# Performance work log

Measured on AMD Instinct MI355X. Metric: run time of the kernel, lower is better.

The kernel has to match this reference:

```python
import jax, jax.numpy as jnp
import numpy as np


def _lstm_layer(x, h0, c0, w_ih, w_hh, b):
    """x: [T,B,I], h0/c0: [B,H], w_ih: [4H,I], w_hh: [4H,H], b: [4H]. PyTorch gate order i,f,g,o."""
    H = h0.shape[-1]
    # Precompute input projection for all timesteps in one big GEMM.
    xg = jnp.einsum('tbi,gi->tbg', x, w_ih) + b  # [T,B,4H]

    def step(carry, xg_t):
        h, c = carry
        g = xg_t + h @ w_hh.T  # [B,4H]
        i, f, gg, o = jnp.split(g, 4, axis=-1)
        c_new = jax.nn.sigmoid(f) * c + jax.nn.sigmoid(i) * jnp.tanh(gg)
        h_new = jax.nn.sigmoid(o) * jnp.tanh(c_new)
        return (h_new, c_new), h_new

    (_, _), hs = jax.lax.scan(step, (h0, c0), xg)
    return hs  # [T,B,H]


def setup_inputs() -> dict:
    key = jax.random.key(0)
    ks = jax.random.split(key, 12)
    T, B, I, H, O, L = 2048, 32, 256, 512, 1024, 2
    s = 1.0 / np.sqrt(H)  # PyTorch LSTM init scale
    return {
        'x': jax.random.normal(ks[0], (T, B, I), jnp.float32),
        'h0': jnp.zeros((L, B, H), jnp.float32),
        'c0': jnp.zeros((L, B, H), jnp.float32),
        'w_ih0': jax.random.normal(ks[1], (4 * H, I), jnp.float32) * s,
        'w_hh0': jax.random.normal(ks[2], (4 * H, H), jnp.float32) * s,
        'b_ih0': jax.random.normal(ks[3], (4 * H,), jnp.float32) * s,
        'b_hh0': jax.random.normal(ks[4], (4 * H,), jnp.float32) * s,
        'w_ih1': jax.random.normal(ks[5], (4 * H, H), jnp.float32) * s,
        'w_hh1': jax.random.normal(ks[6], (4 * H, H), jnp.float32) * s,
        'b_ih1': jax.random.normal(ks[7], (4 * H,), jnp.float32) * s,
        'b_hh1': jax.random.normal(ks[8], (4 * H,), jnp.float32) * s,
        'fc_w': jax.random.normal(ks[9], (O, H), jnp.float32) * s,
        'fc_b': jax.random.normal(ks[10], (O,), jnp.float32) * s,
    }


def reference(x, h0, c0, w_ih0, w_hh0, b_ih0, b_hh0, w_ih1, w_hh1, b_ih1, b_hh1, fc_w, fc_b):
    h1 = _lstm_layer(x, h0[0], c0[0], w_ih0, w_hh0, b_ih0 + b_hh0)   # [T,B,H]
    h2 = _lstm_layer(h1, h0[1], c0[1], w_ih1, w_hh1, b_ih1 + b_hh1)  # [T,B,H]
    logits = h2[-1] @ fc_w.T + fc_b  # out[-1] -> fc, [B,O]
    return jax.nn.log_softmax(logits, axis=1)
```

## Files before the change

### kernel.cpp

```cpp
#include <hip/hip_runtime.h>
#include <stdint.h>

#define TT 2048
#define BB 32
#define II 256
#define HH 512
#define OO 1024
#define NWGL 64
#define NWG 128
#define RING 32

typedef __attribute__((ext_vector_type(8))) short short8;
typedef __attribute__((ext_vector_type(4))) float floatx4;

__device__ __forceinline__ unsigned short f2bf(float f) {
  union { float f; unsigned u; } v; v.f = f;
  unsigned r = v.u + 0x7FFFu + ((v.u >> 16) & 1u);
  return (unsigned short)(r >> 16);
}
__device__ __forceinline__ float bf2f(unsigned short b) {
  union { float f; unsigned u; } v; v.u = ((unsigned)b) << 16; return v.f;
}
__device__ __forceinline__ float sigmf(float x) { return 1.0f / (1.0f + __expf(-x)); }
__device__ __forceinline__ float tanhfast(float x) {
  float xc = fminf(fmaxf(x, -15.f), 15.f);
  float e = __expf(2.f * xc);
  return (e - 1.f) / (e + 1.f);
}

#define LD1(d, va, IMM)                                                     \
  asm volatile("global_load_dwordx4 %0, %1, off offset:" IMM " sc0 sc1"     \
               : "=v"(d) : "v"(va) : "memory")
#define LD1C(d, va, IMM)                                                    \
  asm volatile("global_load_dwordx4 %0, %1, off offset:" IMM                \
               : "=v"(d) : "v"(va) : "memory")

#define ISSUE8(dst, va) do {                                                \
    LD1(dst[0], va, "0");   LD1(dst[1], va, "64");                          \
    LD1(dst[2], va, "128"); LD1(dst[3], va, "192");                         \
    LD1(dst[4], va, "256"); LD1(dst[5], va, "320");                         \
    LD1(dst[6], va, "384"); LD1(dst[7], va, "448"); } while (0)
#define ISSUE8C(dst, va) do {                                               \
    LD1C(dst[0], va, "0");   LD1C(dst[1], va, "64");                        \
    LD1C(dst[2], va, "128"); LD1C(dst[3], va, "192");                       \
    LD1C(dst[4], va, "256"); LD1C(dst[5], va, "320");                       \
    LD1C(dst[6], va, "384"); LD1C(dst[7], va, "448"); } while (0)

#define WAITV(N) do {                                                       \
    asm volatile("s_waitcnt vmcnt(" #N ")" ::: "memory");                   \
    __builtin_amdgcn_sched_barrier(0); } while (0)

#define MF8(tt_, src, wbase) do {                                           \
    _Pragma("unroll")                                                       \
    for (int j = 0; j < 8; j++) {                                           \
      acc[0][tt_] = __builtin_amdgcn_mfma_f32_16x16x32_bf16(src[j], wf[0][(wbase) + j], acc[0][tt_], 0, 0, 0); \
      acc[1][tt_] = __builtin_amdgcn_mfma_f32_16x16x32_bf16(src[j], wf[1][(wbase) + j], acc[1][tt_], 0, 0, 0); \
    } } while (0)

#define PROGREAD(dst, addr64)                                               \
  asm volatile("global_load_dword %0, %1, off sc0 sc1"                      \
               : "=v"(dst) : "v"(addr64) : "memory")

#define BARRIER(gcnt, root, gen, target, do_poll) do {                      \
  if (lane == 0) {                                                          \
    int prev = __hip_atomic_fetch_add(gcnt, 1, __ATOMIC_RELAXED, __HIP_MEMORY_SCOPE_AGENT); \
    if (prev == 8 * (target) - 1) {                                         \
      int p2 = __hip_atomic_fetch_add(root, 1, __ATOMIC_RELAXED, __HIP_MEMORY_SCOPE_AGENT); \
      if (p2 == 8 * (target) - 1) {                                         \
        __hip_atomic_store(gen, (target), __ATOMIC_RELAXED, __HIP_MEMORY_SCOPE_AGENT); \
      } else if (do_poll) {                                                 \
        while (__hip_atomic_load(gen, __ATOMIC_RELAXED, __HIP_MEMORY_SCOPE_AGENT) < (target)) \
          __builtin_amdgcn_s_sleep(1);                                      \
      }                                                                     \
    } else if (do_poll) {                                                   \
      while (__hip_atomic_load(gen, __ATOMIC_RELAXED, __HIP_MEMORY_SCOPE_AGENT) < (target)) \
        __builtin_amdgcn_s_sleep(1);                                        \
    }                                                                       \
  } } while (0)

#define TAIL(hwaddr) do {                                                   \
  _Pragma("unroll")                                                         \
  for (int tau = 0; tau < 2; tau++) {                                       \
    _Pragma("unroll")                                                       \
    for (int tt = 0; tt < 2; tt++) {                                        \
      _Pragma("unroll")                                                     \
      for (int r = 0; r < 4; r++) {                                         \
        float val = acc[tau][tt][r];                                        \
        float nl = (gate == 2) ? tanhfast(val) : sigmf(val);                \
        int base2 = (lane & 48) | u;                                        \
        float iv = __shfl(nl, base2);                                       \
        float fv = __shfl(nl, base2 | 4);                                   \
        float gv = __shfl(nl, base2 | 8);                                   \
        float ov = __shfl(nl, base2 | 12);                                  \
        if (gate == 0) {                                                    \
          float cn = fv * cst[tau][tt][r] + iv * gv;                        \
          cst[tau][tt][r] = cn;                                             \
          float hn = ov * tanhfast(cn);                                     \
          int b = tt * 16 + krow * 4 + r;                                   \
          sh[b][tau * 4 + u] = f2bf(hn);                                    \
        }                                                                   \
      }                                                                     \
    }                                                                       \
  }                                                                         \
  asm volatile("s_waitcnt lgkmcnt(0)" ::: "memory");                        \
  __builtin_amdgcn_sched_barrier(0);                                        \
  if (lane < 32) {                                                          \
    short8 v = *reinterpret_cast<const short8*>(&sh[lane][0]);              \
    unsigned long long sa = (hwaddr) + stoff;                               \
    asm volatile("global_store_dwordx4 %0, %1, off sc0 sc1"                 \
                 :: "v"(sa), "v"(v) : "memory");                            \
  } } while (0)

__global__ void k_convert_x(const float* __restrict__ x, ushort* __restrict__ xb, int n4) {
  int i = blockIdx.x * blockDim.x + threadIdx.x;
  int stride = gridDim.x * blockDim.x;
  const float4* xf = reinterpret_cast<const float4*>(x);
  ushort4* ob = reinterpret_cast<ushort4*>(xb);
  for (; i < n4; i += stride) {
    float4 f = xf[i];
    ushort4 o;
    o.x = f2bf(f.x); o.y = f2bf(f.y); o.z = f2bf(f.z); o.w = f2bf(f.w);
    ob[i] = o;
  }
}

__global__ void k_init(const float* __restrict__ h0in, ushort* __restrict__ ring,
                       ushort* __restrict__ h1b1, int* __restrict__ bar) {
  int i = threadIdx.x;
  ushort* slot31 = ring + (RING - 1) * BB * HH;
  for (int k = i; k < BB * HH; k += blockDim.x) {
    slot31[k] = f2bf(h0in[k]);
    h1b1[k]   = f2bf(h0in[BB * HH + k]);
  }
  for (int k = i; k < 1024; k += blockDim.x) bar[k] = 0;
}

__global__ __launch_bounds__(64, 1) void k_lstm(
    const ushort* __restrict__ xb,
    const float* __restrict__ w_ih0, const float* __restrict__ w_hh0,
    const float* __restrict__ b_ih0, const float* __restrict__ b_hh0,
    const float* __restrict__ w_ih1, const float* __restrict__ w_hh1,
    const float* __restrict__ b_ih1, const float* __restrict__ b_hh1,
    const float* __restrict__ c0in,
    ushort* __restrict__ ring,
    ushort* __restrict__ h1b0, ushort* __restrict__ h1b1,
    int* __restrict__ bar)
{
  __shared__ ushort sh[BB][8];
  const int wg = blockIdx.x;
  const int lane = threadIdx.x;
  const bool isL0 = wg < NWGL;
  const int g = isL0 ? wg : wg - NWGL;
  const int col = lane & 15;
  const int krow = lane >> 4;
  const int u = col & 3;
  const int gate = col >> 2;

  short8 wf[2][32];
#define LOADW(dst, base, rowlen, kbase, tau) do {                             \
    const int _grow = gate * HH + g * 8 + (tau) * 4 + u;                      \
    const float* _p = (base) + (size_t)_grow * (rowlen) + (kbase) + krow * 8; \
    short8 _r;                                                                \
    _Pragma("unroll")                                                         \
    for (int _j = 0; _j < 8; _j++) _r[_j] = (short)f2bf(_p[_j]);              \
    (dst) = _r; } while (0)

  if (isL0) {
#pragma unroll
    for (int tau = 0; tau < 2; tau++) {
#pragma unroll
      for (int kk = 0; kk < 8; kk++)  LOADW(wf[tau][kk],      w_ih0, II, kk * 32, tau);
#pragma unroll
      for (int kk = 0; kk < 16; kk++) LOADW(wf[tau][8 + kk],  w_hh0, HH, kk * 32, tau);
    }
  } else {
#pragma unroll
    for (int tau = 0; tau < 2; tau++) {
#pragma unroll
      for (int kk = 0; kk < 16; kk++) LOADW(wf[tau][kk],      w_ih1, HH, kk * 32, tau);
#pragma unroll
      for (int kk = 0; kk < 16; kk++) LOADW(wf[tau][16 + kk], w_hh1, HH, kk * 32, tau);
    }
  }
  float bias[2];
#pragma unroll
  for (int tau = 0; tau < 2; tau++) {
    const int grow = gate * HH + g * 8 + tau * 4 + u;
    bias[tau] = isL0 ? (b_ih0[grow] + b_hh0[grow]) : (b_ih1[grow] + b_hh1[grow]);
  }

  float cst[2][2][4];
  {
    const float* cbase = c0in + (isL0 ? 0 : 1) * BB * HH;
#pragma unroll
    for (int tau = 0; tau < 2; tau++)
#pragma unroll
      for (int tt = 0; tt < 2; tt++)
#pragma unroll
        for (int r = 0; r < 4; r++) {
          int b = tt * 16 + krow * 4 + r;
          cst[tau][tt][r] = cbase[b * HH + g * 8 + tau * 4 + u];
        }
  }

  int* gcnt = bar + (isL0 ? 0 : 320) + (g >> 3) * 32;
  int* root = bar + (isL0 ? 256 : 576);
  int* gen  = bar + (isL0 ? 288 : 608);
  const unsigned long long genOther =
      (unsigned long long)(bar + (isL0 ? 608 : 288));

  const int vo00 = col * 1024 + krow * 16;
  const unsigned long long stoff = (unsigned long long)(lane * 1024 + g * 16);
  ushort* h1bufs[2] = { h1b0, h1b1 };

  short8 wa[8], wb[8], wc[8], wd[8];
  floatx4 acc[2][2];
  const floatx4 bi0 = (floatx4){ bias[0], bias[0], bias[0], bias[0] };
  const floatx4 bi1 = (floatx4){ bias[1], bias[1], bias[1], bias[1] };

  if (isL0) {
    const unsigned long long xbase = (unsigned long long)xb + (col * 512 + krow * 16);
    int seen1 = 0;
    for (int t = 0; t < TT; ++t) {
      if (((t & 7) == 0) && t >= 32) {
        while (seen1 < t - 24) {
          int sv; PROGREAD(sv, genOther); WAITV(0); seen1 = sv;
          if (seen1 < t - 24) __builtin_amdgcn_s_sleep(8);
        }
      }
      acc[0][0] = bi0; acc[0][1] = bi0; acc[1][0] = bi1; acc[1][1] = bi1;
      const unsigned long long ha =
          (unsigned long long)ring + ((t + RING - 1) & (RING - 1)) * (BB * HH * 2) + vo00;
      const unsigned long long xa = xbase + (unsigned long long)t * (BB * II * 2);
      ISSUE8(wa, ha); ISSUE8(wb, ha + 512); ISSUE8(wc, ha + 16384); ISSUE8(wd, ha + 16896);
      WAITV(24); MF8(0, wa, 8);  ISSUE8C(wa, xa);
      WAITV(24); MF8(0, wb, 16); ISSUE8C(wb, xa + 8192);
      WAITV(24); MF8(1, wc, 8);
      WAITV(16); MF8(1, wd, 16);
      WAITV(8);  MF8(0, wa, 0);
      WAITV(0);  MF8(1, wb, 0);
      const unsigned long long hw =
          (unsigned long long)ring + (t & (RING - 1)) * (BB * HH * 2);
      TAIL(hw);
      WAITV(0);
      BARRIER(gcnt, root, gen, t + 1, (t != TT - 1));
    }
  } else {
    int seen0 = 0;
    int sv_next = 0;
    for (int t = 0; t < TT; ++t) {
      acc[0][0] = bi0; acc[0][1] = bi0; acc[1][0] = bi1; acc[1][1] = bi1;
      const unsigned long long h1a =
          (unsigned long long)h1bufs[(t + 1) & 1] + vo00;
      ISSUE8(wa, h1a); ISSUE8(wb, h1a + 512); ISSUE8(wc, h1a + 16384); ISSUE8(wd, h1a + 16896);
      if (seen0 < t + 1) {
        while (true) {
          int sv; PROGREAD(sv, genOther); WAITV(0); seen0 = sv;
          if (seen0 >= t + 1) break;
          __builtin_amdgcn_s_sleep(8);
        }
      }
      const unsigned long long h0a =
          (unsigned long long)ring + (t & (RING - 1)) * (BB * HH * 2) + vo00;
      WAITV(24); MF8(0, wa, 16); ISSUE8(wa, h0a);
      WAITV(24); MF8(0, wb, 24); ISSUE8(wb, h0a + 512);
      WAITV(24); MF8(1, wc, 16); ISSUE8(wc, h0a + 16384);
      WAITV(24); MF8(1, wd, 24); ISSUE8(wd, h0a + 16896);
      WAITV(24); MF8(0, wa, 0);
      WAITV(16); MF8(0, wb, 8);
      WAITV(8);  MF8(1, wc, 0);
      WAITV(0);  MF8(1, wd, 8);
      const unsigned long long hw = (unsigned long long)h1bufs[t & 1];
      TAIL(hw);
      PROGREAD(sv_next, genOther);
      WAITV(0);
      seen0 = (sv_next > seen0) ? sv_next : seen0;
      if (t != TT - 1) BARRIER(gcnt, root, gen, t + 1, true);
    }
  }
}

__global__ __launch_bounds__(256) void k_fc(const ushort* __restrict__ h1,
                                            const float* __restrict__ fcw,
                                            const float* __restrict__ fcb,
                                            float* __restrict__ out) {
  __shared__ float hsh[HH];
  __shared__ float red[256];
  const int b = blockIdx.x, tid = threadIdx.x;
  for (int k = tid; k < HH; k += 256) hsh[k] = bf2f(h1[b * HH + k]);
  __syncthreads();
  float lg[4];
#pragma unroll
  for (int q = 0; q < 4; q++) {
    int o = q * 256 + tid;
    float acc = fcb[o];
    const float* wr = fcw + (size_t)o * HH;
#pragma unroll 4
    for (int k = 0; k < HH; k += 4) {
      float4 w4 = *reinterpret_cast<const float4*>(wr + k);
      acc += hsh[k] * w4.x + hsh[k + 1] * w4.y + hsh[k + 2] * w4.z + hsh[k + 3] * w4.w;
    }
    lg[q] = acc;
  }
  float m = fmaxf(fmaxf(lg[0], lg[1]), fmaxf(lg[2], lg[3]));
  red[tid] = m; __syncthreads();
  for (int s = 128; s > 0; s >>= 1) { if (tid < s) red[tid] = fmaxf(red[tid], red[tid + s]); __syncthreads(); }
  m = red[0]; __syncthreads();
  float se = 0.f;
#pragma unroll
  for (int q = 0; q < 4; q++) se += __expf(lg[q] - m);
  red[tid] = se; __syncthreads();
  for (int s = 128; s > 0; s >>= 1) { if (tid < s) red[tid] += red[tid + s]; __syncthreads(); }
  float lse = m + logf(red[0]);
#pragma unroll
  for (int q = 0; q < 4; q++) out[b * OO + q * 256 + tid] = lg[q] - lse;
}

extern "C" void kernel_launch(void* const* d_in, const int* in_sizes, int n_in,
                              void* d_out, int out_size, void* d_ws, size_t ws_size,
                              hipStream_t stream) {
  const float* x     = (const float*)d_in[0];
  const float* h0    = (const float*)d_in[1];
  const float* c0    = (const float*)d_in[2];
  const float* w_ih0 = (const float*)d_in[3];
  const float* w_hh0 = (const float*)d_in[4];
  const float* b_ih0 = (const float*)d_in[5];
  const float* b_hh0 = (const float*)d_in[6];
  const float* w_ih1 = (const float*)d_in[7];
  const float* w_hh1 = (const float*)d_in[8];
  const float* b_ih1 = (const float*)d_in[9];
  const float* b_hh1 = (const float*)d_in[10];
  const float* fcw   = (const float*)d_in[11];
  const float* fcb   = (const float*)d_in[12];
  float* out = (float*)d_out;

  char* ws = (char*)d_ws;
  size_t off = 0;
  ushort* xb   = (ushort*)(ws + off); off += (size_t)TT * BB * II * 2;
  ushort* ring = (ushort*)(ws + off); off += (size_t)RING * BB * HH * 2;
  ushort* h1b0 = (ushort*)(ws + off); off += BB * HH * 2;
  ushort* h1b1 = (ushort*)(ws + off); off += BB * HH * 2;
  int* bar = (int*)(ws + off); off += 1024 * sizeof(int);

  k_convert_x<<<2048, 256, 0, stream>>>(x, xb, TT * BB * II / 4);
  k_init<<<1, 256, 0, stream>>>(h0, ring, h1b1, bar);
  k_lstm<<<NWG, 64, 0, stream>>>(xb, w_ih0, w_hh0, b_ih0, b_hh0,
                                 w_ih1, w_hh1, b_ih1, b_hh1, c0,
                                 ring, h1b0, h1b1, bar);
  k_fc<<<BB, 256, 0, stream>>>(h1b1, fcw, fcb, out);
}
```

Baseline: 16.12 ms.

## Replace hierarchical atomic grid barriers with per-slot sequence flags

Drops the two-level atomic counter barrier each layer used at every timestep. Each workgroup now publishes a per-slot sequence number after writing its slice of h, and consumers poll all 64 producer flags with one wide load and a wave vote. Layer 1 also gets a ring buffer for its hidden state, and its progress is reported per workgroup so layer 0 can throttle. This removes the serialized atomic fetch-adds and the gen broadcast from the critical path. In exchange every wave spins on 64 flags, and the memory-ordering guarantees now rest on sc0 sc1 stores.

Result: slower. 16.87 ms (+4.7%).

```diff
diff --git a/kernel.cpp b/kernel.cpp
--- a/kernel.cpp
+++ b/kernel.cpp
@@ -9,6 +9,7 @@
 #define NWGL 64
 #define NWG 128
 #define RING 32
+#define SLOTB (BB * HH * 2)
 
 typedef __attribute__((ext_vector_type(8))) short short8;
 typedef __attribute__((ext_vector_type(4))) float floatx4;
@@ -61,22 +62,14 @@
   asm volatile("global_load_dword %0, %1, off sc0 sc1"                      \
                : "=v"(dst) : "v"(addr64) : "memory")
 
-#define BARRIER(gcnt, root, gen, target, do_poll) do {                      \
-  if (lane == 0) {                                                          \
-    int prev = __hip_atomic_fetch_add(gcnt, 1, __ATOMIC_RELAXED, __HIP_MEMORY_SCOPE_AGENT); \
-    if (prev == 8 * (target) - 1) {                                         \
-      int p2 = __hip_atomic_fetch_add(root, 1, __ATOMIC_RELAXED, __HIP_MEMORY_SCOPE_AGENT); \
-      if (p2 == 8 * (target) - 1) {                                         \
-        __hip_atomic_store(gen, (target), __ATOMIC_RELAXED, __HIP_MEMORY_SCOPE_AGENT); \
-      } else if (do_poll) {                                                 \
-        while (__hip_atomic_load(gen, __ATOMIC_RELAXED, __HIP_MEMORY_SCOPE_AGENT) < (target)) \
-          __builtin_amdgcn_s_sleep(1);                                      \
-      }                                                                     \
-    } else if (do_poll) {                                                   \
-      while (__hip_atomic_load(gen, __ATOMIC_RELAXED, __HIP_MEMORY_SCOPE_AGENT) < (target)) \
-        __builtin_amdgcn_s_sleep(1);                                        \
-    }                                                                       \
-  } } while (0)
+#define SEQSTORE(arr, slot, val) do {                                       \
+    if (lane == 0) {                                                        \
+      unsigned long long _a = (unsigned long long)(arr) +                   \
+          (unsigned long long)((slot) * 64 + g) * 4;                        \
+      int _v = (val);                                                       \
+      asm volatile("global_store_dword %0, %1, off sc0 sc1"                 \
+                   :: "v"(_a), "v"(_v) : "memory");                         \
+    } } while (0)
 
 #define TAIL(hwaddr) do {                                                   \
   _Pragma("unroll")                                                         \
@@ -124,15 +117,23 @@
   }
 }
 
-__global__ void k_init(const float* __restrict__ h0in, ushort* __restrict__ ring,
-                       ushort* __restrict__ h1b1, int* __restrict__ bar) {
+__global__ void k_init(const float* __restrict__ h0in,
+                       ushort* __restrict__ h0ring, ushort* __restrict__ h1ring,
+                       int* __restrict__ h0seq, int* __restrict__ h1seq,
+                       int* __restrict__ pr1) {
   int i = threadIdx.x;
-  ushort* slot31 = ring + (RING - 1) * BB * HH;
+  ushort* s0 = h0ring + (RING - 1) * BB * HH;
+  ushort* s1 = h1ring + (RING - 1) * BB * HH;
   for (int k = i; k < BB * HH; k += blockDim.x) {
-    slot31[k] = f2bf(h0in[k]);
-    h1b1[k]   = f2bf(h0in[BB * HH + k]);
-  }
-  for (int k = i; k < 1024; k += blockDim.x) bar[k] = 0;
+    s0[k] = f2bf(h0in[k]);
+    s1[k] = f2bf(h0in[BB * HH + k]);
+  }
+  for (int k = i; k < RING * 64; k += blockDim.x) {
+    int v = (k >= (RING - 1) * 64) ? -1 : (int)0x80000000;
+    h0seq[k] = v;
+    h1seq[k] = v;
+  }
+  for (int k = i; k < 64; k += blockDim.x) pr1[k] = -1;
 }
 
 __global__ __launch_bounds__(64, 1) void k_lstm(
@@ -142,9 +143,9 @@
     const float* __restrict__ w_ih1, const float* __restrict__ w_hh1,
     const float* __restrict__ b_ih1, const float* __restrict__ b_hh1,
     const float* __restrict__ c0in,
-    ushort* __restrict__ ring,
-    ushort* __restrict__ h1b0, ushort* __restrict__ h1b1,
-    int* __restrict__ bar)
+    ushort* __restrict__ h0ring, ushort* __restrict__ h1ring,
+    int* __restrict__ h0seq, int* __restrict__ h1seq,
+    int* __restrict__ pr1)
 {
   __shared__ ushort sh[BB][8];
   const int wg = blockIdx.x;
@@ -203,15 +204,10 @@
         }
   }
 
-  int* gcnt = bar + (isL0 ? 0 : 320) + (g >> 3) * 32;
-  int* root = bar + (isL0 ? 256 : 576);
-  int* gen  = bar + (isL0 ? 288 : 608);
-  const unsigned long long genOther =
-      (unsigned long long)(bar + (isL0 ? 608 : 288));
-
+  const unsigned long long h0rb = (unsigned long long)h0ring;
+  const unsigned long long h1rb = (unsigned long long)h1ring;
   const int vo00 = col * 1024 + krow * 16;
   const unsigned long long stoff = (unsigned long long)(lane * 1024 + g * 16);
-  ushort* h1bufs[2] = { h1b0, h1b1 };
 
   short8 wa[8], wb[8], wc[8], wd[8];
   floatx4 acc[2][2];
@@ -220,17 +216,24 @@
 
   if (isL0) {
     const unsigned long long xbase = (unsigned long long)xb + (col * 512 + krow * 16);
-    int seen1 = 0;
     for (int t = 0; t < TT; ++t) {
+      {
+        const unsigned long long sa = (unsigned long long)h0seq +
+            (unsigned long long)(((t + 31) & 31) * 64 + lane) * 4;
+        int sv; PROGREAD(sv, sa); WAITV(0);
+        while (!__all(sv == t - 1)) {
+          __builtin_amdgcn_s_sleep(1); PROGREAD(sv, sa); WAITV(0);
+        }
+      }
       if (((t & 7) == 0) && t >= 32) {
-        while (seen1 < t - 24) {
-          int sv; PROGREAD(sv, genOther); WAITV(0); seen1 = sv;
-          if (seen1 < t - 24) __builtin_amdgcn_s_sleep(8);
+        const unsigned long long pa = (unsigned long long)pr1 + lane * 4ull;
+        int pv; PROGREAD(pv, pa); WAITV(0);
+        while (!__all(pv >= t - 24)) {
+          __builtin_amdgcn_s_sleep(4); PROGREAD(pv, pa); WAITV(0);
         }
       }
       acc[0][0] = bi0; acc[0][1] = bi0; acc[1][0] = bi1; acc[1][1] = bi1;
-      const unsigned long long ha =
-          (unsigned long long)ring + ((t + RING - 1) & (RING - 1)) * (BB * HH * 2) + vo00;
+      const unsigned long long ha = h0rb + (unsigned long long)((t + 31) & 31) * SLOTB + vo00;
       const unsigned long long xa = xbase + (unsigned long long)t * (BB * II * 2);
       ISSUE8(wa, ha); ISSUE8(wb, ha + 512); ISSUE8(wc, ha + 16384); ISSUE8(wd, ha + 16896);
       WAITV(24); MF8(0, wa, 8);  ISSUE8C(wa, xa);
@@ -239,43 +242,44 @@
       WAITV(16); MF8(1, wd, 16);
       WAITV(8);  MF8(0, wa, 0);
       WAITV(0);  MF8(1, wb, 0);
-      const unsigned long long hw =
-          (unsigned long long)ring + (t & (RING - 1)) * (BB * HH * 2);
-      TAIL(hw);
+      TAIL(h0rb + (unsigned long long)(t & 31) * SLOTB);
       WAITV(0);
-      BARRIER(gcnt, root, gen, t + 1, (t != TT - 1));
+      SEQSTORE(h0seq, (t & 31), t);
     }
   } else {
-    int seen0 = 0;
-    int sv_next = 0;
     for (int t = 0; t < TT; ++t) {
-      acc[0][0] = bi0; acc[0][1] = bi0; acc[1][0] = bi1; acc[1][1] = bi1;
-      const unsigned long long h1a =
-          (unsigned long long)h1bufs[(t + 1) & 1] + vo00;
-      ISSUE8(wa, h1a); ISSUE8(wb, h1a + 512); ISSUE8(wc, h1a + 16384); ISSUE8(wd, h1a + 16896);
-      if (seen0 < t + 1) {
-        while (true) {
-          int sv; PROGREAD(sv, genOther); WAITV(0); seen0 = sv;
-          if (seen0 >= t + 1) break;
-          __builtin_amdgcn_s_sleep(8);
+      {
+        const unsigned long long sa0 = (unsigned long long)h0seq +
+            (unsigned long long)((t & 31) * 64 + lane) * 4;
+        const unsigned long long sa1 = (unsigned long long)h1seq +
+            (unsigned long long)(((t + 31) & 31) * 64 + lane) * 4;
+        int s0, s1; PROGREAD(s0, sa0); PROGREAD(s1, sa1); WAITV(0);
+        while (!(__all(s0 == t) & __all(s1 == t - 1))) {
+          __builtin_amdgcn_s_sleep(1);
+          PROGREAD(s0, sa0); PROGREAD(s1, sa1); WAITV(0);
         }
       }
-      const unsigned long long h0a =
-          (unsigned long long)ring + (t & (RING - 1)) * (BB * HH * 2) + vo00;
-      WAITV(24); MF8(0, wa, 16); ISSUE8(wa, h0a);
-      WAITV(24); MF8(0, wb, 24); ISSUE8(wb, h0a + 512);
-      WAITV(24); MF8(1, wc, 16); ISSUE8(wc, h0a + 16384);
-      WAITV(24); MF8(1, wd, 24); ISSUE8(wd, h0a + 16896);
-      WAITV(24); MF8(0, wa, 0);
-      WAITV(16); MF8(0, wb, 8);
-      WAITV(8);  MF8(1, wc, 0);
-      WAITV(0);  MF8(1, wd, 8);
-      const unsigned long long hw = (unsigned long long)h1bufs[t & 1];
-      TAIL(hw);
-      PROGREAD(sv_next, genOther);
+      acc[0][0] = bi0; acc[0][1] = bi0; acc[1][0] = bi1; acc[1][1] = bi1;
+      const unsigned long long a0 = h0rb + (unsigned long long)(t & 31) * SLOTB + vo00;
+      const unsigned long long a1 = h1rb + (unsigned long long)((t + 31) & 31) * SLOTB + vo00;
+      ISSUE8(wa, a0); ISSUE8(wb, a0 + 512); ISSUE8(wc, a0 + 16384); ISSUE8(wd, a0 + 16896);
+      WAITV(24); MF8(0, wa, 0); ISSUE8(wa, a1);
+      WAITV(24); MF8(0, wb, 8); ISSUE8(wb, a1 + 512);
+      WAITV(24); MF8(1, wc, 0); ISSUE8(wc, a1 + 16384);
+      WAITV(24); MF8(1, wd, 8); ISSUE8(wd, a1 + 16896);
+      WAITV(24); MF8(0, wa, 16);
+      WAITV(16); MF8(0, wb, 24);
+      WAITV(8);  MF8(1, wc, 16);
+      WAITV(0);  MF8(1, wd, 24);
+      if (lane == 0) {
+        unsigned long long pa = (unsigned long long)pr1 + (unsigned long long)g * 4;
+        int pv = t;
+        asm volatile("global_store_dword %0, %1, off sc0 sc1"
+                     :: "v"(pa), "v"(pv) : "memory");
+      }
+      TAIL(h1rb + (unsigned long long)(t & 31) * SLOTB);
       WAITV(0);
-      seen0 = (sv_next > seen0) ? sv_next : seen0;
-      if (t != TT - 1) BARRIER(gcnt, root, gen, t + 1, true);
+      SEQSTORE(h1seq, (t & 31), t);
     }
   }
 }
@@ -336,16 +340,17 @@
 
   char* ws = (char*)d_ws;
   size_t off = 0;
-  ushort* xb   = (ushort*)(ws + off); off += (size_t)TT * BB * II * 2;
-  ushort* ring = (ushort*)(ws + off); off += (size_t)RING * BB * HH * 2;
-  ushort* h1b0 = (ushort*)(ws + off); off += BB * HH * 2;
-  ushort* h1b1 = (ushort*)(ws + off); off += BB * HH * 2;
-  int* bar = (int*)(ws + off); off += 1024 * sizeof(int);
+  ushort* xb     = (ushort*)(ws + off); off += (size_t)TT * BB * II * 2;
+  ushort* h0ring = (ushort*)(ws + off); off += (size_t)RING * BB * HH * 2;
+  ushort* h1ring = (ushort*)(ws + off); off += (size_t)RING * BB * HH * 2;
+  int* h0seq = (int*)(ws + off); off += RING * 64 * sizeof(int);
+  int* h1seq = (int*)(ws + off); off += RING * 64 * sizeof(int);
+  int* pr1   = (int*)(ws + off); off += 64 * sizeof(int);
 
   k_convert_x<<<2048, 256, 0, stream>>>(x, xb, TT * BB * II / 4);
-  k_init<<<1, 256, 0, stream>>>(h0, ring, h1b1, bar);
+  k_init<<<1, 256, 0, stream>>>(h0, h0ring, h1ring, h0seq, h1seq, pr1);
   k_lstm<<<NWG, 64, 0, stream>>>(xb, w_ih0, w_hh0, b_ih0, b_hh0,
                                  w_ih1, w_hh1, b_ih1, b_hh1, c0,
-                                 ring, h1b0, h1b1, bar);
-  k_fc<<<BB, 256, 0, stream>>>(h1b1, fcw, fcb, out);
-}
+                                 h0ring, h1ring, h0seq, h1seq, pr1);
+  k_fc<<<BB, 256, 0, stream>>>(h1ring + (RING - 1) * BB * HH, fcw, fcb, out);
+}
```
